# Kernel optimization log

Hardware: AMD Instinct MI355X
Metric: run time of the kernel (lower is better)

Reference implementation:

```python
import jax, jax.numpy as jnp
import numpy as np

N = 100000      # num_nodes
E = 1600000     # num_edges (avg degree 16)
IN = 128        # in_feats
OUT = 64        # out_feats
D = 4           # num_divisions


def setup_inputs() -> dict:
    key = jax.random.key(0)
    ks = jax.random.split(key, 6)
    feature = jax.random.normal(ks[0], (N, IN), dtype=jnp.float32)
    # per-division linear weights, stored as [D, out, in] (torch Linear layout)
    W = jax.random.normal(ks[1], (D, OUT, IN), dtype=jnp.float32) * (1.0 / np.sqrt(IN))
    norm = jax.random.uniform(ks[2], (N, 1), dtype=jnp.float32)
    src = jax.random.randint(ks[3], (E,), 0, N)
    dst = jax.random.randint(ks[4], (E,), 0, N)
    edge_div = jax.random.randint(ks[5], (E,), 0, D)
    return {"feature": feature, "W": W, "norm": norm,
            "src": src, "dst": dst, "edge_div": edge_div}


def reference(feature, W, norm, src, dst, edge_div):
    # Per-division linear transform + per-node norm scaling: [D, N, OUT]
    t = jnp.einsum('ni,doi->dno', feature, W) * norm
    # Gather the source-node features for each edge from its division's transform
    msgs = t[edge_div, src]                      # [E, OUT]
    # Scatter-sum to (dst, division) slots in one segment_sum pass
    seg = dst * D + edge_div                     # [E]
    agg = jax.ops.segment_sum(msgs, seg, num_segments=N * D)  # [N*D, OUT]
    # Row order is node-major, division-minor -> reshape == torch.cat over divisions
    h = agg.reshape(N, D * OUT) * norm           # final norm scale
    return jax.nn.relu(h)
```

## Files before the change

kernel.cpp:

```cpp
#include <hip/hip_runtime.h>


#define IN_F   128
#define OUTC   256
#define EPC    4096
#define NBMAX  512
#define STGF   5120
#define GEMM_GRID 512

typedef __bf16 bf16x8 __attribute__((ext_vector_type(8)));
typedef float  f32x4  __attribute__((ext_vector_type(4)));

__device__ inline float bf16_to_f32(unsigned short h) {
    return __uint_as_float(((unsigned int)h) << 16);
}

__device__ inline void split_bf16x8(const float4 q0, const float4 q1,
                                    bf16x8& h, bf16x8& l)
{
    float av[8] = {q0.x, q0.y, q0.z, q0.w, q1.x, q1.y, q1.z, q1.w};
    #pragma unroll
    for (int i = 0; i < 8; ++i) {
        const __bf16 hb = (__bf16)av[i];
        h[i] = hb;
        l[i] = (__bf16)(av[i] - (float)hb);
    }
}

__global__ __launch_bounds__(256) void wpack_kernel(
    const float* __restrict__ W, bf16x8* __restrict__ Bpack)
{
    const int idx  = blockIdx.x * 256 + threadIdx.x;
    const int lane = idx & 63;
    const int c    = (idx >> 6) & 15;
    const int s    = idx >> 10;
    const int col  = c * 16 + (lane & 15);
    const int k0   = s * 32 + (lane >> 4) * 8;
    const float* p = W + col * IN_F + k0;
    bf16x8 h, l;
    #pragma unroll
    for (int e = 0; e < 8; ++e) {
        const float v = p[e];
        const __bf16 hb = (__bf16)v;
        h[e] = hb;
        l[e] = (__bf16)(v - (float)hb);
    }
    Bpack[idx]        = h;
    Bpack[4096 + idx] = l;
}

__global__ __launch_bounds__(256, 2) void gemm_mfma_kernel(
    const float* __restrict__ feat, const bf16x8* __restrict__ Bpack,
    const float* __restrict__ norm, __bf16* __restrict__ t,
    int nNodes, int nTiles)
{
    const int tid  = threadIdx.x;
    const int wid  = tid >> 6;
    const int lane = tid & 63;
    const int r    = lane & 15;
    const int g    = lane >> 4;
    const int c0   = wid << 2;

    bf16x8 bfh[4][4], bfl[4][4];
    #pragma unroll
    for (int s = 0; s < 4; ++s)
        #pragma unroll
        for (int cc = 0; cc < 4; ++cc) {
            bfh[s][cc] = Bpack[(s * 16 + c0 + cc) * 64 + lane];
            bfl[s][cc] = Bpack[4096 + (s * 16 + c0 + cc) * 64 + lane];
        }

    for (int tile = blockIdx.x; tile < nTiles; tile += gridDim.x) {
        const int row0 = tile * 32;
        const int ra0 = min(row0 + r, nNodes - 1);
        const int ra1 = min(row0 + 16 + r, nNodes - 1);
        const float* pa0 = feat + (size_t)ra0 * IN_F;
        const float* pa1 = feat + (size_t)ra1 * IN_F;

        f32x4 acc[2][4];
        #pragma unroll
        for (int h = 0; h < 2; ++h)
            #pragma unroll
            for (int cc = 0; cc < 4; ++cc)
                acc[h][cc] = (f32x4){0.f, 0.f, 0.f, 0.f};

        #pragma unroll
        for (int s = 0; s < 4; ++s) {
            const int koff = s * 32 + g * 8;
            bf16x8 a0h, a0l, a1h, a1l;
            split_bf16x8(*(const float4*)(pa0 + koff),
                         *(const float4*)(pa0 + koff + 4), a0h, a0l);
            split_bf16x8(*(const float4*)(pa1 + koff),
                         *(const float4*)(pa1 + koff + 4), a1h, a1l);
            #pragma unroll
            for (int cc = 0; cc < 4; ++cc) {
                acc[0][cc] = __builtin_amdgcn_mfma_f32_16x16x32_bf16(bfh[s][cc], a0h, acc[0][cc], 0, 0, 0);
                acc[0][cc] = __builtin_amdgcn_mfma_f32_16x16x32_bf16(bfh[s][cc], a0l, acc[0][cc], 0, 0, 0);
                acc[0][cc] = __builtin_amdgcn_mfma_f32_16x16x32_bf16(bfl[s][cc], a0h, acc[0][cc], 0, 0, 0);
                acc[1][cc] = __builtin_amdgcn_mfma_f32_16x16x32_bf16(bfh[s][cc], a1h, acc[1][cc], 0, 0, 0);
                acc[1][cc] = __builtin_amdgcn_mfma_f32_16x16x32_bf16(bfh[s][cc], a1l, acc[1][cc], 0, 0, 0);
                acc[1][cc] = __builtin_amdgcn_mfma_f32_16x16x32_bf16(bfl[s][cc], a1h, acc[1][cc], 0, 0, 0);
            }
        }

        #pragma unroll
        for (int h = 0; h < 2; ++h) {
            const int grow = row0 + (h << 4) + r;
            if (grow >= nNodes) continue;
            const float nm = norm[grow];
            __bf16* po = t + (size_t)grow * OUTC;
            #pragma unroll
            for (int cc = 0; cc < 4; ++cc) {
                union { __bf16 b[4]; uint2 u; } pk;
                #pragma unroll
                for (int q = 0; q < 4; ++q)
                    pk.b[q] = (__bf16)(acc[h][cc][q] * nm);
                *(uint2*)(po + (c0 + cc) * 16 + (g << 2)) = pk.u;
            }
        }
    }
}

__global__ __launch_bounds__(256) void bucket_hist_kernel(
    const int* __restrict__ dst, int* __restrict__ bcnt, int nEdges, int nBuck)
{
    __shared__ int h[NBMAX];
    const int tid = threadIdx.x;
    for (int b = tid; b < nBuck; b += 256) h[b] = 0;
    __syncthreads();
    const int e0 = blockIdx.x * EPC;
    const int cnt = min(EPC, nEdges - e0);
    for (int i = tid; i < cnt; i += 256)
        atomicAdd(&h[((unsigned)dst[e0 + i]) >> 8], 1);
    __syncthreads();
    for (int b = tid; b < nBuck; b += 256)
        if (h[b]) atomicAdd(&bcnt[b], h[b]);
}

__global__ __launch_bounds__(256) void bucket_scan_kernel(
    const int* __restrict__ bcnt, int* __restrict__ bbase,
    int* __restrict__ bfront, int nBuck)
{
    __shared__ int wsum[4], woff[4];
    const int tid = threadIdx.x;
    const int i0 = 2 * tid, i1 = 2 * tid + 1;
    const int h0 = (i0 < nBuck) ? bcnt[i0] : 0;
    const int h1 = (i1 < nBuck) ? bcnt[i1] : 0;
    const int s = h0 + h1;
    int incl = s;
    const int lane = tid & 63;
    #pragma unroll
    for (int off = 1; off < 64; off <<= 1) {
        const int o = __shfl_up(incl, off);
        if (lane >= off) incl += o;
    }
    if (lane == 63) wsum[tid >> 6] = incl;
    __syncthreads();
    if (tid == 0) { int r = 0; for (int i = 0; i < 4; ++i) { woff[i] = r; r += wsum[i]; } }
    __syncthreads();
    const int e = incl - s + woff[tid >> 6];
    if (i0 < nBuck) { bbase[i0] = e;      bfront[i0] = e;      }
    if (i1 < nBuck) { bbase[i1] = e + h0; bfront[i1] = e + h0; }
}

__global__ __launch_bounds__(256) void bucket_place_kernel(
    const int* __restrict__ src, const int* __restrict__ dst,
    const int* __restrict__ ediv, int* __restrict__ bfront,
    uint2* __restrict__ rec, int nEdges, int nBuck)
{
    __shared__ uint2 stg[EPC];
    __shared__ unsigned short stgB[EPC];
    __shared__ int hist[NBMAX], excl[NBMAX], cur[NBMAX], gpos[NBMAX];
    __shared__ int wsum[4], woff[4];

    const int tid = threadIdx.x;
    const int e0 = blockIdx.x * EPC;
    const int cnt = min(EPC, nEdges - e0);

    for (int b = tid; b < nBuck; b += 256) hist[b] = 0;
    __syncthreads();

    for (int i = tid; i < cnt; i += 256)
        atomicAdd(&hist[((unsigned)dst[e0 + i]) >> 8], 1);
    __syncthreads();

    {
        const int i0 = 2 * tid, i1 = 2 * tid + 1;
        const int h0 = (i0 < nBuck) ? hist[i0] : 0;
        const int h1 = (i1 < nBuck) ? hist[i1] : 0;
        const int s = h0 + h1;
        int incl = s;
        const int lane = tid & 63;
        #pragma unroll
        for (int off = 1; off < 64; off <<= 1) {
            const int o = __shfl_up(incl, off);
            if (lane >= off) incl += o;
        }
        if (lane == 63) wsum[tid >> 6] = incl;
        __syncthreads();
        if (tid == 0) { int r = 0; for (int i = 0; i < 4; ++i) { woff[i] = r; r += wsum[i]; } }
        __syncthreads();
        const int e = incl - s + woff[tid >> 6];
        if (i0 < nBuck) { excl[i0] = e;      cur[i0] = e;
                          gpos[i0] = h0 ? atomicAdd(&bfront[i0], h0) : 0; }
        if (i1 < nBuck) { excl[i1] = e + h0; cur[i1] = e + h0;
                          gpos[i1] = h1 ? atomicAdd(&bfront[i1], h1) : 0; }
    }
    __syncthreads();

    for (int i = tid; i < cnt; i += 256) {
        const int e = e0 + i;
        const int d = dst[e];
        const int b = ((unsigned)d) >> 8;
        const int lp = atomicAdd(&cur[b], 1);
        stg[lp]  = make_uint2((unsigned)((src[e] << 2) | ediv[e]), (unsigned)d);
        stgB[lp] = (unsigned short)b;
    }
    __syncthreads();

    for (int s2 = tid; s2 < cnt; s2 += 256) {
        const int b = stgB[s2];
        rec[gpos[b] + (s2 - excl[b])] = stg[s2];
    }
}

__global__ __launch_bounds__(256) void bucket_fine_kernel(
    const uint2* __restrict__ rec, const int* __restrict__ bbase,
    const int* __restrict__ bcnt, int* __restrict__ cursor,
    int* __restrict__ payload, int nNodes)
{
    __shared__ int nhist[256], ncur[256];
    __shared__ int pay[STGF];
    __shared__ int wsum[4], woff[4];

    const int tid = threadIdx.x;
    const int b = blockIdx.x;
    const int base = bbase[b];
    const int cnt = bcnt[b];
    const int node0 = b << 8;

    nhist[tid] = 0;
    __syncthreads();
    for (int i = tid; i < cnt; i += 256)
        atomicAdd(&nhist[rec[base + i].y & 255], 1);
    __syncthreads();

    const int v = nhist[tid];
    int incl = v;
    const int lane = tid & 63;
    #pragma unroll
    for (int off = 1; off < 64; off <<= 1) {
        const int o = __shfl_up(incl, off);
        if (lane >= off) incl += o;
    }
    if (lane == 63) wsum[tid >> 6] = incl;
    __syncthreads();
    if (tid == 0) { int r = 0; for (int i = 0; i < 4; ++i) { woff[i] = r; r += wsum[i]; } }
    __syncthreads();
    incl += woff[tid >> 6];
    ncur[tid] = incl - v;
    if (node0 + tid < nNodes) cursor[node0 + tid] = base + incl;
    __syncthreads();

    if (cnt <= STGF) {
        for (int i = tid; i < cnt; i += 256) {
            const uint2 rr = rec[base + i];
            pay[atomicAdd(&ncur[rr.y & 255], 1)] = (int)rr.x;
        }
        __syncthreads();
        for (int i = tid; i < cnt; i += 256) payload[base + i] = pay[i];
    } else {
        for (int i = tid; i < cnt; i += 256) {
            const uint2 rr = rec[base + i];
            payload[base + atomicAdd(&ncur[rr.y & 255], 1)] = (int)rr.x;
        }
    }
}

__global__ __launch_bounds__(256) void aggregate_kernel(
    const unsigned short* __restrict__ t, const int* __restrict__ cursor,
    const int* __restrict__ payload, const float* __restrict__ norm,
    float* __restrict__ out, int nNodes)
{
    const int wave = (int)((blockIdx.x * 256u + threadIdx.x) >> 6);
    const int lane = threadIdx.x & 63;
    if (wave >= nNodes) return;
    const int e0 = (wave == 0) ? 0 : cursor[wave - 1];
    const int e1 = cursor[wave];

    float acc0 = 0.f, acc1 = 0.f, acc2 = 0.f, acc3 = 0.f;
    int e = e0;
    for (; e + 3 < e1; e += 4) {
        const int p0 = payload[e + 0];
        const int p1 = payload[e + 1];
        const int p2 = payload[e + 2];
        const int p3 = payload[e + 3];
        const float v0 = bf16_to_f32(t[(size_t)(p0 >> 2) * OUTC + (p0 & 3) * 64 + lane]);
        const float v1 = bf16_to_f32(t[(size_t)(p1 >> 2) * OUTC + (p1 & 3) * 64 + lane]);
        const float v2 = bf16_to_f32(t[(size_t)(p2 >> 2) * OUTC + (p2 & 3) * 64 + lane]);
        const float v3 = bf16_to_f32(t[(size_t)(p3 >> 2) * OUTC + (p3 & 3) * 64 + lane]);
        const int d0 = p0 & 3, d1 = p1 & 3, d2 = p2 & 3, d3 = p3 & 3;
        acc0 += (d0 == 0 ? v0 : 0.f) + (d1 == 0 ? v1 : 0.f) + (d2 == 0 ? v2 : 0.f) + (d3 == 0 ? v3 : 0.f);
        acc1 += (d0 == 1 ? v0 : 0.f) + (d1 == 1 ? v1 : 0.f) + (d2 == 1 ? v2 : 0.f) + (d3 == 1 ? v3 : 0.f);
        acc2 += (d0 == 2 ? v0 : 0.f) + (d1 == 2 ? v1 : 0.f) + (d2 == 2 ? v2 : 0.f) + (d3 == 2 ? v3 : 0.f);
        acc3 += (d0 == 3 ? v0 : 0.f) + (d1 == 3 ? v1 : 0.f) + (d2 == 3 ? v2 : 0.f) + (d3 == 3 ? v3 : 0.f);
    }
    for (; e < e1; ++e) {
        const int p0 = payload[e];
        const float v0 = bf16_to_f32(t[(size_t)(p0 >> 2) * OUTC + (p0 & 3) * 64 + lane]);
        const int d0 = p0 & 3;
        acc0 += (d0 == 0 ? v0 : 0.f);
        acc1 += (d0 == 1 ? v0 : 0.f);
        acc2 += (d0 == 2 ? v0 : 0.f);
        acc3 += (d0 == 3 ? v0 : 0.f);
    }

    const float nm = norm[wave];
    float* po = out + (size_t)wave * OUTC;
    po[0 * 64 + lane] = fmaxf(acc0 * nm, 0.f);
    po[1 * 64 + lane] = fmaxf(acc1 * nm, 0.f);
    po[2 * 64 + lane] = fmaxf(acc2 * nm, 0.f);
    po[3 * 64 + lane] = fmaxf(acc3 * nm, 0.f);
}

extern "C" void kernel_launch(void* const* d_in, const int* in_sizes, int n_in,
                              void* d_out, int out_size, void* d_ws, size_t ws_size,
                              hipStream_t stream) {
    const float* feat = (const float*)d_in[0];
    const float* W    = (const float*)d_in[1];
    const float* norm = (const float*)d_in[2];
    const int*   src  = (const int*)d_in[3];
    const int*   dst  = (const int*)d_in[4];
    const int*   ediv = (const int*)d_in[5];
    float* out = (float*)d_out;

    const int nNodes = in_sizes[0] / IN_F;
    const int nEdges = in_sizes[3];
    const int nBuck  = (nNodes + 255) >> 8;
    const int nChunk = (nEdges + EPC - 1) / EPC;
    const int nTiles = (nNodes + 31) / 32;

    char* ws = (char*)d_ws;
    const size_t t_bytes      = (size_t)nNodes * OUTC * sizeof(unsigned short);
    const size_t rec_bytes    = (size_t)nEdges * sizeof(uint2);
    const size_t pay_bytes    = (size_t)nEdges * sizeof(int);
    const size_t cursor_bytes = (size_t)nNodes * sizeof(int);
    const size_t bp_bytes     = 8192 * sizeof(bf16x8);

    __bf16* t      = (__bf16*)ws;
    uint2*  rec    = (uint2*)(ws + t_bytes);
    int*    payload= (int*)(ws + t_bytes + rec_bytes);
    int*    cursor = (int*)(ws + t_bytes + rec_bytes + pay_bytes);
    bf16x8* Bpack  = (bf16x8*)(ws + t_bytes + rec_bytes + pay_bytes + cursor_bytes);
    int*    bcnt   = (int*)(ws + t_bytes + rec_bytes + pay_bytes + cursor_bytes + bp_bytes);
    int*    bbase  = bcnt + NBMAX;
    int*    bfront = bcnt + 2 * NBMAX;
    (void)ws_size; (void)out_size; (void)n_in;

    hipMemsetAsync(bcnt, 0, nBuck * sizeof(int), stream);
    wpack_kernel<<<16, 256, 0, stream>>>(W, Bpack);
    bucket_hist_kernel<<<nChunk, 256, 0, stream>>>(dst, bcnt, nEdges, nBuck);
    bucket_scan_kernel<<<1, 256, 0, stream>>>(bcnt, bbase, bfront, nBuck);
    bucket_place_kernel<<<nChunk, 256, 0, stream>>>(src, dst, ediv, bfront, rec,
                                                    nEdges, nBuck);
    bucket_fine_kernel<<<nBuck, 256, 0, stream>>>(rec, bbase, bcnt, cursor, payload,
                                                  nNodes);
    gemm_mfma_kernel<<<GEMM_GRID, 256, 0, stream>>>(feat, Bpack, norm, t,
                                                    nNodes, nTiles);
    aggregate_kernel<<<(nNodes + 3) / 4, 256, 0, stream>>>((const unsigned short*)t,
                                                           cursor, payload, norm,
                                                           out, nNodes);
}
```

Before: 335.8 us.

## Sort edges by (dst,division) bins and pre-split normalized features to bf16

Records now pack src, the low dst byte and the division into one 32-bit word, and the fine sort bins by (node,division). This lets aggregation sum four contiguous segments with no per-edge division masking, and it halves record bandwidth. A new pre-pass scales features by norm and splits them into bf16 hi/lo arrays so the GEMM loads bf16 directly. The GEMM moves ahead of the sort so the split arrays can alias the record workspace. The trade is an extra full pass over the features, and the packing caps src below 2^22 nodes.

```diff
diff --git a/kernel.cpp b/kernel.cpp
--- a/kernel.cpp
+++ b/kernel.cpp
@@ -13,18 +13,6 @@
 
 __device__ inline float bf16_to_f32(unsigned short h) {
     return __uint_as_float(((unsigned int)h) << 16);
-}
-
-__device__ inline void split_bf16x8(const float4 q0, const float4 q1,
-                                    bf16x8& h, bf16x8& l)
-{
-    float av[8] = {q0.x, q0.y, q0.z, q0.w, q1.x, q1.y, q1.z, q1.w};
-    #pragma unroll
-    for (int i = 0; i < 8; ++i) {
-        const __bf16 hb = (__bf16)av[i];
-        h[i] = hb;
-        l[i] = (__bf16)(av[i] - (float)hb);
-    }
 }
 
 __global__ __launch_bounds__(256) void wpack_kernel(
@@ -49,9 +37,30 @@
     Bpack[4096 + idx] = l;
 }
 
+__global__ __launch_bounds__(256) void featsplit_kernel(
+    const float* __restrict__ feat, const float* __restrict__ norm,
+    __bf16* __restrict__ fhi, __bf16* __restrict__ flo, int total4)
+{
+    int i = blockIdx.x * 256 + threadIdx.x;
+    if (i >= total4) return;
+    const int row = i >> 5;
+    const float nm = norm[row];
+    const float4 v = ((const float4*)feat)[i];
+    const float x[4] = {v.x * nm, v.y * nm, v.z * nm, v.w * nm};
+    union { __bf16 b[4]; uint2 u; } hi, lo;
+    #pragma unroll
+    for (int j = 0; j < 4; ++j) {
+        const __bf16 hb = (__bf16)x[j];
+        hi.b[j] = hb;
+        lo.b[j] = (__bf16)(x[j] - (float)hb);
+    }
+    ((uint2*)fhi)[i] = hi.u;
+    ((uint2*)flo)[i] = lo.u;
+}
+
 __global__ __launch_bounds__(256, 2) void gemm_mfma_kernel(
-    const float* __restrict__ feat, const bf16x8* __restrict__ Bpack,
-    const float* __restrict__ norm, __bf16* __restrict__ t,
+    const __bf16* __restrict__ fhi, const __bf16* __restrict__ flo,
+    const bf16x8* __restrict__ Bpack, __bf16* __restrict__ t,
     int nNodes, int nTiles)
 {
     const int tid  = threadIdx.x;
@@ -74,8 +83,10 @@
         const int row0 = tile * 32;
         const int ra0 = min(row0 + r, nNodes - 1);
         const int ra1 = min(row0 + 16 + r, nNodes - 1);
-        const float* pa0 = feat + (size_t)ra0 * IN_F;
-        const float* pa1 = feat + (size_t)ra1 * IN_F;
+        const __bf16* ph0 = fhi + (size_t)ra0 * IN_F;
+        const __bf16* pl0 = flo + (size_t)ra0 * IN_F;
+        const __bf16* ph1 = fhi + (size_t)ra1 * IN_F;
+        const __bf16* pl1 = flo + (size_t)ra1 * IN_F;
 
         f32x4 acc[2][4];
         #pragma unroll
@@ -87,11 +98,10 @@
         #pragma unroll
         for (int s = 0; s < 4; ++s) {
             const int koff = s * 32 + g * 8;
-            bf16x8 a0h, a0l, a1h, a1l;
-            split_bf16x8(*(const float4*)(pa0 + koff),
-                         *(const float4*)(pa0 + koff + 4), a0h, a0l);
-            split_bf16x8(*(const float4*)(pa1 + koff),
-                         *(const float4*)(pa1 + koff + 4), a1h, a1l);
+            const bf16x8 a0h = *(const bf16x8*)(ph0 + koff);
+            const bf16x8 a0l = *(const bf16x8*)(pl0 + koff);
+            const bf16x8 a1h = *(const bf16x8*)(ph1 + koff);
+            const bf16x8 a1l = *(const bf16x8*)(pl1 + koff);
             #pragma unroll
             for (int cc = 0; cc < 4; ++cc) {
                 acc[0][cc] = __builtin_amdgcn_mfma_f32_16x16x32_bf16(bfh[s][cc], a0h, acc[0][cc], 0, 0, 0);
@@ -107,14 +117,13 @@
         for (int h = 0; h < 2; ++h) {
             const int grow = row0 + (h << 4) + r;
             if (grow >= nNodes) continue;
-            const float nm = norm[grow];
             __bf16* po = t + (size_t)grow * OUTC;
             #pragma unroll
             for (int cc = 0; cc < 4; ++cc) {
                 union { __bf16 b[4]; uint2 u; } pk;
                 #pragma unroll
                 for (int q = 0; q < 4; ++q)
-                    pk.b[q] = (__bf16)(acc[h][cc][q] * nm);
+                    pk.b[q] = (__bf16)acc[h][cc][q];
                 *(uint2*)(po + (c0 + cc) * 16 + (g << 2)) = pk.u;
             }
         }
@@ -166,9 +175,9 @@
 __global__ __launch_bounds__(256) void bucket_place_kernel(
     const int* __restrict__ src, const int* __restrict__ dst,
     const int* __restrict__ ediv, int* __restrict__ bfront,
-    uint2* __restrict__ rec, int nEdges, int nBuck)
-{
-    __shared__ uint2 stg[EPC];
+    unsigned int* __restrict__ rec, int nEdges, int nBuck)
+{
+    __shared__ unsigned int stg[EPC];
     __shared__ unsigned short stgB[EPC];
     __shared__ int hist[NBMAX], excl[NBMAX], cur[NBMAX], gpos[NBMAX];
     __shared__ int wsum[4], woff[4];
@@ -210,10 +219,10 @@
 
     for (int i = tid; i < cnt; i += 256) {
         const int e = e0 + i;
-        const int d = dst[e];
-        const int b = ((unsigned)d) >> 8;
+        const unsigned d = (unsigned)dst[e];
+        const int b = d >> 8;
         const int lp = atomicAdd(&cur[b], 1);
-        stg[lp]  = make_uint2((unsigned)((src[e] << 2) | ediv[e]), (unsigned)d);
+        stg[lp]  = ((unsigned)src[e] << 10) | ((d & 255u) << 2) | (unsigned)ediv[e];
         stgB[lp] = (unsigned short)b;
     }
     __syncthreads();
@@ -225,11 +234,11 @@
 }
 
 __global__ __launch_bounds__(256) void bucket_fine_kernel(
-    const uint2* __restrict__ rec, const int* __restrict__ bbase,
-    const int* __restrict__ bcnt, int* __restrict__ cursor,
+    const unsigned int* __restrict__ rec, const int* __restrict__ bbase,
+    const int* __restrict__ bcnt, int* __restrict__ cursor4,
     int* __restrict__ payload, int nNodes)
 {
-    __shared__ int nhist[256], ncur[256];
+    __shared__ int nhist[1024], ncur[1024];
     __shared__ int pay[STGF];
     __shared__ int wsum[4], woff[4];
 
@@ -237,16 +246,19 @@
     const int b = blockIdx.x;
     const int base = bbase[b];
     const int cnt = bcnt[b];
-    const int node0 = b << 8;
-
-    nhist[tid] = 0;
+    const int bin0 = b << 10;
+    const int nBins = nNodes * 4;
+
+    #pragma unroll
+    for (int j = 0; j < 4; ++j) nhist[tid + j * 256] = 0;
     __syncthreads();
     for (int i = tid; i < cnt; i += 256)
-        atomicAdd(&nhist[rec[base + i].y & 255], 1);
-    __syncthreads();
-
-    const int v = nhist[tid];
-    int incl = v;
+        atomicAdd(&nhist[rec[base + i] & 1023u], 1);
+    __syncthreads();
+
+    const int4 h4 = *(const int4*)&nhist[tid << 2];
+    const int s = h4.x + h4.y + h4.z + h4.w;
+    int incl = s;
     const int lane = tid & 63;
     #pragma unroll
     for (int off = 1; off < 64; off <<= 1) {
@@ -257,70 +269,77 @@
     __syncthreads();
     if (tid == 0) { int r = 0; for (int i = 0; i < 4; ++i) { woff[i] = r; r += wsum[i]; } }
     __syncthreads();
-    incl += woff[tid >> 6];
-    ncur[tid] = incl - v;
-    if (node0 + tid < nNodes) cursor[node0 + tid] = base + incl;
+    const int ebase = incl - s + woff[tid >> 6];
+    const int p1 = ebase + h4.x;
+    const int p2 = p1 + h4.y;
+    const int p3 = p2 + h4.z;
+    const int p4 = p3 + h4.w;
+    ncur[(tid << 2) + 0] = ebase;
+    ncur[(tid << 2) + 1] = p1;
+    ncur[(tid << 2) + 2] = p2;
+    ncur[(tid << 2) + 3] = p3;
+    {
+        const int gb = bin0 + (tid << 2);
+        if (gb + 0 < nBins) cursor4[gb + 0] = base + p1;
+        if (gb + 1 < nBins) cursor4[gb + 1] = base + p2;
+        if (gb + 2 < nBins) cursor4[gb + 2] = base + p3;
+        if (gb + 3 < nBins) cursor4[gb + 3] = base + p4;
+    }
     __syncthreads();
 
     if (cnt <= STGF) {
         for (int i = tid; i < cnt; i += 256) {
-            const uint2 rr = rec[base + i];
-            pay[atomicAdd(&ncur[rr.y & 255], 1)] = (int)rr.x;
+            const unsigned int rr = rec[base + i];
+            pay[atomicAdd(&ncur[rr & 1023u], 1)] = (int)(rr >> 10);
         }
         __syncthreads();
         for (int i = tid; i < cnt; i += 256) payload[base + i] = pay[i];
     } else {
         for (int i = tid; i < cnt; i += 256) {
-            const uint2 rr = rec[base + i];
-            payload[base + atomicAdd(&ncur[rr.y & 255], 1)] = (int)rr.x;
-        }
-    }
+            const unsigned int rr = rec[base + i];
+            payload[base + atomicAdd(&ncur[rr & 1023u], 1)] = (int)(rr >> 10);
+        }
+    }
+}
+
+__device__ inline float seg_sum(const unsigned short* __restrict__ tp,
+                                const int* __restrict__ payload,
+                                int& e, const int end)
+{
+    float a = 0.f, b = 0.f;
+    for (; e + 1 < end; e += 2) {
+        const int s0 = payload[e];
+        const int s1 = payload[e + 1];
+        a += bf16_to_f32(tp[(size_t)s0 << 8]);
+        b += bf16_to_f32(tp[(size_t)s1 << 8]);
+    }
+    if (e < end) { a += bf16_to_f32(tp[(size_t)payload[e] << 8]); ++e; }
+    return a + b;
 }
 
 __global__ __launch_bounds__(256) void aggregate_kernel(
-    const unsigned short* __restrict__ t, const int* __restrict__ cursor,
+    const unsigned short* __restrict__ t, const int* __restrict__ cursor4,
     const int* __restrict__ payload, const float* __restrict__ norm,
     float* __restrict__ out, int nNodes)
 {
     const int wave = (int)((blockIdx.x * 256u + threadIdx.x) >> 6);
     const int lane = threadIdx.x & 63;
     if (wave >= nNodes) return;
-    const int e0 = (wave == 0) ? 0 : cursor[wave - 1];
-    const int e1 = cursor[wave];
-
-    float acc0 = 0.f, acc1 = 0.f, acc2 = 0.f, acc3 = 0.f;
-    int e = e0;
-    for (; e + 3 < e1; e += 4) {
-        const int p0 = payload[e + 0];
-        const int p1 = payload[e + 1];
-        const int p2 = payload[e + 2];
-        const int p3 = payload[e + 3];
-        const float v0 = bf16_to_f32(t[(size_t)(p0 >> 2) * OUTC + (p0 & 3) * 64 + lane]);
-        const float v1 = bf16_to_f32(t[(size_t)(p1 >> 2) * OUTC + (p1 & 3) * 64 + lane]);
-        const float v2 = bf16_to_f32(t[(size_t)(p2 >> 2) * OUTC + (p2 & 3) * 64 + lane]);
-        const float v3 = bf16_to_f32(t[(size_t)(p3 >> 2) * OUTC + (p3 & 3) * 64 + lane]);
-        const int d0 = p0 & 3, d1 = p1 & 3, d2 = p2 & 3, d3 = p3 & 3;
-        acc0 += (d0 == 0 ? v0 : 0.f) + (d1 == 0 ? v1 : 0.f) + (d2 == 0 ? v2 : 0.f) + (d3 == 0 ? v3 : 0.f);
-        acc1 += (d0 == 1 ? v0 : 0.f) + (d1 == 1 ? v1 : 0.f) + (d2 == 1 ? v2 : 0.f) + (d3 == 1 ? v3 : 0.f);
-        acc2 += (d0 == 2 ? v0 : 0.f) + (d1 == 2 ? v1 : 0.f) + (d2 == 2 ? v2 : 0.f) + (d3 == 2 ? v3 : 0.f);
-        acc3 += (d0 == 3 ? v0 : 0.f) + (d1 == 3 ? v1 : 0.f) + (d2 == 3 ? v2 : 0.f) + (d3 == 3 ? v3 : 0.f);
-    }
-    for (; e < e1; ++e) {
-        const int p0 = payload[e];
-        const float v0 = bf16_to_f32(t[(size_t)(p0 >> 2) * OUTC + (p0 & 3) * 64 + lane]);
-        const int d0 = p0 & 3;
-        acc0 += (d0 == 0 ? v0 : 0.f);
-        acc1 += (d0 == 1 ? v0 : 0.f);
-        acc2 += (d0 == 2 ? v0 : 0.f);
-        acc3 += (d0 == 3 ? v0 : 0.f);
-    }
+    const int idx4 = wave << 2;
+    const int4 ends = *(const int4*)(cursor4 + idx4);
+    int e = idx4 ? cursor4[idx4 - 1] : 0;
+
+    const float a0 = seg_sum(t + lane,       payload, e, ends.x);
+    const float a1 = seg_sum(t + 64 + lane,  payload, e, ends.y);
+    const float a2 = seg_sum(t + 128 + lane, payload, e, ends.z);
+    const float a3 = seg_sum(t + 192 + lane, payload, e, ends.w);
 
     const float nm = norm[wave];
     float* po = out + (size_t)wave * OUTC;
-    po[0 * 64 + lane] = fmaxf(acc0 * nm, 0.f);
-    po[1 * 64 + lane] = fmaxf(acc1 * nm, 0.f);
-    po[2 * 64 + lane] = fmaxf(acc2 * nm, 0.f);
-    po[3 * 64 + lane] = fmaxf(acc3 * nm, 0.f);
+    po[0 * 64 + lane] = fmaxf(a0 * nm, 0.f);
+    po[1 * 64 + lane] = fmaxf(a1 * nm, 0.f);
+    po[2 * 64 + lane] = fmaxf(a2 * nm, 0.f);
+    po[3 * 64 + lane] = fmaxf(a3 * nm, 0.f);
 }
 
 extern "C" void kernel_launch(void* const* d_in, const int* in_sizes, int n_in,
@@ -341,33 +360,39 @@
     const int nTiles = (nNodes + 31) / 32;
 
     char* ws = (char*)d_ws;
-    const size_t t_bytes      = (size_t)nNodes * OUTC * sizeof(unsigned short);
-    const size_t rec_bytes    = (size_t)nEdges * sizeof(uint2);
+    const size_t t_bytes  = (size_t)nNodes * OUTC * sizeof(__bf16);
+    const size_t f_bytes  = (size_t)nNodes * IN_F * sizeof(__bf16);
+    const size_t rec_bytes    = (size_t)nEdges * sizeof(unsigned);
     const size_t pay_bytes    = (size_t)nEdges * sizeof(int);
-    const size_t cursor_bytes = (size_t)nNodes * sizeof(int);
     const size_t bp_bytes     = 8192 * sizeof(bf16x8);
 
-    __bf16* t      = (__bf16*)ws;
-    uint2*  rec    = (uint2*)(ws + t_bytes);
-    int*    payload= (int*)(ws + t_bytes + rec_bytes);
-    int*    cursor = (int*)(ws + t_bytes + rec_bytes + pay_bytes);
-    bf16x8* Bpack  = (bf16x8*)(ws + t_bytes + rec_bytes + pay_bytes + cursor_bytes);
-    int*    bcnt   = (int*)(ws + t_bytes + rec_bytes + pay_bytes + cursor_bytes + bp_bytes);
+    __bf16* t   = (__bf16*)ws;
+    char*   r2  = ws + t_bytes;
+    __bf16* fhi = (__bf16*)r2;
+    __bf16* flo = (__bf16*)(r2 + f_bytes);
+    unsigned* rec     = (unsigned*)r2;
+    int*      payload = (int*)(r2 + rec_bytes);
+    int*      cursor4 = (int*)(r2 + rec_bytes + pay_bytes);
+    bf16x8* Bpack = (bf16x8*)(r2 + 2 * f_bytes);
+    int*    bcnt  = (int*)(r2 + 2 * f_bytes + bp_bytes);
     int*    bbase  = bcnt + NBMAX;
     int*    bfront = bcnt + 2 * NBMAX;
     (void)ws_size; (void)out_size; (void)n_in;
 
     hipMemsetAsync(bcnt, 0, nBuck * sizeof(int), stream);
     wpack_kernel<<<16, 256, 0, stream>>>(W, Bpack);
+    const int total4 = nNodes * (IN_F / 4);
+    featsplit_kernel<<<(total4 + 255) / 256, 256, 0, stream>>>(feat, norm, fhi, flo,
+                                                               total4);
+    gemm_mfma_kernel<<<GEMM_GRID, 256, 0, stream>>>(fhi, flo, Bpack, t,
+                                                    nNodes, nTiles);
     bucket_hist_kernel<<<nChunk, 256, 0, stream>>>(dst, bcnt, nEdges, nBuck);
     bucket_scan_kernel<<<1, 256, 0, stream>>>(bcnt, bbase, bfront, nBuck);
     bucket_place_kernel<<<nChunk, 256, 0, stream>>>(src, dst, ediv, bfront, rec,
                                                     nEdges, nBuck);
-    bucket_fine_kernel<<<nBuck, 256, 0, stream>>>(rec, bbase, bcnt, cursor, payload,
+    bucket_fine_kernel<<<nBuck, 256, 0, stream>>>(rec, bbase, bcnt, cursor4, payload,
                                                   nNodes);
-    gemm_mfma_kernel<<<GEMM_GRID, 256, 0, stream>>>(feat, Bpack, norm, t,
-                                                    nNodes, nTiles);
     aggregate_kernel<<<(nNodes + 3) / 4, 256, 0, stream>>>((const unsigned short*)t,
-                                                           cursor, payload, norm,
+                                                           cursor4, payload, norm,
                                                            out, nNodes);
 }
```

New measurement: 381.8 us. +13.7%, slower.
